# Performance work log

Measured on AMD Instinct MI355X. Metric: run time of the kernel, lower is better.

Reference implementation:

```python
import jax, jax.numpy as jnp
import numpy as np

B, N, L, D = 256, 128, 2048, 64
ATOM_V, AMINO_V = 2000, 10000
LAYER_GNN, LAYER_CNN, LAYER_OUT = 3, 3, 2
SIDE = 5
WINDOW = 2 * SIDE + 1   # 11 -> conv kernel 23x23, padding 11
N_OUT = 2
EPS = 1e-6


def setup_inputs() -> dict:
    ks = jax.random.split(jax.random.key(0), 16)
    s = 0.05
    return {
        "atoms": jax.random.randint(ks[0], (B, N), 0, ATOM_V),
        "atoms_mask": jnp.ones((B, N), jnp.float32),
        "adjacency": jax.random.uniform(ks[1], (B, N, N), jnp.float32),
        "amino": jax.random.randint(ks[2], (B, L), 0, AMINO_V),
        "amino_mask": jnp.ones((B, L), jnp.float32),
        "emb_fp": jax.random.normal(ks[3], (ATOM_V, D), jnp.float32) * s,
        "emb_word": jax.random.normal(ks[4], (AMINO_V, D), jnp.float32) * s,
        "W_gnn": jax.random.normal(ks[5], (LAYER_GNN, D, D), jnp.float32) * s,
        "b_gnn": jax.random.normal(ks[6], (LAYER_GNN, D), jnp.float32) * s,
        "conv_k": jax.random.normal(ks[7], (LAYER_CNN, 2 * WINDOW + 1, 2 * WINDOW + 1), jnp.float32) * s,
        "conv_b": jax.random.normal(ks[8], (LAYER_CNN,), jnp.float32) * s,
        "W_att": jax.random.normal(ks[9], (D, D), jnp.float32) * s,
        "b_att": jax.random.normal(ks[10], (D,), jnp.float32) * s,
        "W_out": jax.random.normal(ks[11], (LAYER_OUT, 2 * D, 2 * D), jnp.float32) * s,
        "b_out": jax.random.normal(ks[12], (LAYER_OUT, 2 * D), jnp.float32) * s,
        "W_int": jax.random.normal(ks[13], (N_OUT, 2 * D), jnp.float32) * s,
        "b_int": jax.random.normal(ks[14], (N_OUT,), jnp.float32) * s,
    }


def reference(atoms, atoms_mask, adjacency, amino, amino_mask,
              emb_fp, emb_word, W_gnn, b_gnn, conv_k, conv_b,
              W_att, b_att, W_out, b_out, W_int, b_int):
    # ---- compound vector via GNN over dense adjacency ----
    xs = emb_fp[atoms]                                   # [B,N,D]
    for i in range(LAYER_GNN):
        hs = jax.nn.relu(jnp.einsum('bnd,ed->bne', xs, W_gnn[i]) + b_gnn[i])
        xs = xs + jnp.einsum('bnm,bmd->bnd', adjacency, hs)
    am = atoms_mask[..., None]                           # [B,N,1]
    compound = (jnp.sum(xs * am, axis=1) / (jnp.sum(am, axis=1) + EPS))[:, None, :]  # [B,1,D]

    # ---- protein vector via attention-CNN ----
    ps = emb_word[amino][:, None]                        # [B,1,L,D] (NCHW)
    for i in range(LAYER_CNN):
        y = jax.lax.conv_general_dilated(
            ps, conv_k[i][None, None], (1, 1),
            [(WINDOW, WINDOW), (WINDOW, WINDOW)],
            dimension_numbers=('NCHW', 'OIHW', 'NCHW'))
        ps = jax.nn.relu(y + conv_b[i])
    ps = ps[:, 0]                                        # [B,L,D]
    h = jax.nn.relu(jnp.einsum('bqd,ed->bqe', compound, W_att) + b_att)  # [B,1,D]
    hs = jax.nn.relu(jnp.einsum('bld,ed->ble', ps, W_att) + b_att)       # [B,L,D]
    pm = amino_mask[..., None]                           # [B,L,1]
    hs = hs * pm
    weights = jnp.tanh(jnp.einsum('bqd,bld->bql', h, hs))  # [B,1,L]
    ys = jnp.transpose(weights, (0, 2, 1)) * hs             # [B,L,D]
    protein = (jnp.sum(ys, axis=1) / (jnp.sum(pm, axis=1) + EPS))[:, None, :]  # [B,1,D]

    # ---- fuse and predict ----
    cat = jnp.concatenate([compound, protein], axis=2)[:, 0]  # [B,2D]
    for j in range(LAYER_OUT):
        cat = jax.nn.relu(cat @ W_out[j].T + b_out[j])  # dropout is identity in eval
    return cat @ W_int.T + b_int                          # [B,N_OUT]
```

## Files before the change

kernel.cpp:

```cpp
#include <hip/hip_runtime.h>
#include <hip/hip_bf16.h>
#include <cstdint>
#include <cstddef>

#define BB 256
#define NN 128
#define LL 2048
#define DD 64
#define KS 23
#define CPAD 12
#define EPSF 1e-6f
#define ACH 8

typedef __bf16 v8bf __attribute__((ext_vector_type(8)));
typedef float v4f __attribute__((ext_vector_type(4)));

__device__ __forceinline__ float bf2f(uint32_t u) {
  union { uint32_t i; float f; } c; c.i = u << 16; return c.f;
}
__device__ __forceinline__ uint16_t f2bf(float f) {
  union { float f; uint32_t i; } c; c.f = f;
  uint32_t i = c.i;
  return (uint16_t)((i + 0x7fffu + ((i >> 16) & 1u)) >> 16);
}
__device__ __forceinline__ v8bf cvt8(float4 f0, float4 f1) {
  v8bf r;
  r[0] = (__bf16)f0.x; r[1] = (__bf16)f0.y; r[2] = (__bf16)f0.z; r[3] = (__bf16)f0.w;
  r[4] = (__bf16)f1.x; r[5] = (__bf16)f1.y; r[6] = (__bf16)f1.z; r[7] = (__bf16)f1.w;
  return r;
}

#define XSS 68
#define HTS3 136

__global__ __launch_bounds__(256) void gnn_kernel(
    const int* __restrict__ atoms, const float* __restrict__ atoms_mask,
    const float* __restrict__ adj, const float* __restrict__ emb_fp,
    const float* __restrict__ W_gnn, const float* __restrict__ b_gnn,
    const float* __restrict__ W_att, const float* __restrict__ b_att,
    const float* __restrict__ conv_k, uint16_t* __restrict__ btab,
    float* __restrict__ compound, float* __restrict__ hvec_g)
{
  __shared__ float xs[NN * XSS];
  __shared__ uint16_t hsT[DD * HTS3];
  __shared__ float mask_s[NN];
  __shared__ float psum[4][64];
  __shared__ float cvec[64];

  const int b = blockIdx.x;
  const int tid = threadIdx.x;
  const int lane = tid & 63;
  const int w = tid >> 6;
  const int m16 = lane & 15;
  const int s = lane >> 4;

  for (int idx = tid; idx < NN * 16; idx += 256) {
    int n = idx >> 4, c4 = idx & 15;
    int a = atoms[b * NN + n];
    float4 v = ((const float4*)(emb_fp + (size_t)a * DD))[c4];
    *(float4*)(xs + n * XSS + c4 * 4) = v;
  }
  if (tid < NN) mask_s[tid] = atoms_mask[b * NN + tid];
  __syncthreads();

  const int row0 = 32 * w;
  for (int layer = 0; layer < 3; ++layer) {
    v8bf Wf[2][4];
    float bias[4];
    const float* Wl = W_gnn + (size_t)layer * DD * DD;
    #pragma unroll
    for (int nt = 0; nt < 4; ++nt) {
      bias[nt] = b_gnn[layer * DD + nt * 16 + m16];
      #pragma unroll
      for (int kc = 0; kc < 2; ++kc) {
        const float* p = Wl + (size_t)(nt * 16 + m16) * DD + kc * 32 + s * 8;
        Wf[kc][nt] = cvt8(((const float4*)p)[0], ((const float4*)p)[1]);
      }
    }
    float4 araw[8][2];
    const float* adjw = adj + ((size_t)b * NN + row0) * NN;
    #pragma unroll
    for (int kc = 0; kc < 4; ++kc)
      #pragma unroll
      for (int mt = 0; mt < 2; ++mt) {
        const float* p = adjw + (size_t)(mt * 16 + m16) * NN + kc * 32 + s * 8;
        araw[kc * 2 + mt][0] = ((const float4*)p)[0];
        araw[kc * 2 + mt][1] = ((const float4*)p)[1];
      }

    v4f acc[2][4];
    #pragma unroll
    for (int mt = 0; mt < 2; ++mt)
      #pragma unroll
      for (int nt = 0; nt < 4; ++nt)
        acc[mt][nt] = (v4f){bias[nt], bias[nt], bias[nt], bias[nt]};
    #pragma unroll
    for (int kc = 0; kc < 2; ++kc) {
      v8bf Axs[2];
      #pragma unroll
      for (int mt = 0; mt < 2; ++mt) {
        const float* p = xs + (size_t)(row0 + mt * 16 + m16) * XSS + kc * 32 + s * 8;
        Axs[mt] = cvt8(((const float4*)p)[0], ((const float4*)p)[1]);
      }
      #pragma unroll
      for (int mt = 0; mt < 2; ++mt)
        #pragma unroll
        for (int nt = 0; nt < 4; ++nt)
          acc[mt][nt] = __builtin_amdgcn_mfma_f32_16x16x32_bf16(
              Axs[mt], Wf[kc][nt], acc[mt][nt], 0, 0, 0);
    }
    __syncthreads();
    #pragma unroll
    for (int mt = 0; mt < 2; ++mt)
      #pragma unroll
      for (int nt = 0; nt < 4; ++nt) {
        int e = nt * 16 + m16;
        int m = row0 + mt * 16 + s * 4;
        union { uint64_t u; __bf16 h[4]; } pk;
        #pragma unroll
        for (int r = 0; r < 4; ++r)
          pk.h[r] = (__bf16)fmaxf(acc[mt][nt][r], 0.f);
        *(uint64_t*)(hsT + (size_t)e * HTS3 + m) = pk.u;
      }
    __syncthreads();

    v4f acc2[2][4];
    #pragma unroll
    for (int mt = 0; mt < 2; ++mt)
      #pragma unroll
      for (int nt = 0; nt < 4; ++nt)
        #pragma unroll
        for (int r = 0; r < 4; ++r)
          acc2[mt][nt][r] = xs[(size_t)(row0 + mt * 16 + s * 4 + r) * XSS + nt * 16 + m16];
    #pragma unroll
    for (int kc = 0; kc < 4; ++kc) {
      v8bf Aa[2];
      #pragma unroll
      for (int mt = 0; mt < 2; ++mt)
        Aa[mt] = cvt8(araw[kc * 2 + mt][0], araw[kc * 2 + mt][1]);
      v8bf Bh[4];
      #pragma unroll
      for (int nt = 0; nt < 4; ++nt)
        Bh[nt] = *(const v8bf*)(hsT + (size_t)(nt * 16 + m16) * HTS3 + kc * 32 + s * 8);
      #pragma unroll
      for (int mt = 0; mt < 2; ++mt)
        #pragma unroll
        for (int nt = 0; nt < 4; ++nt)
          acc2[mt][nt] = __builtin_amdgcn_mfma_f32_16x16x32_bf16(
              Aa[mt], Bh[nt], acc2[mt][nt], 0, 0, 0);
    }
    #pragma unroll
    for (int mt = 0; mt < 2; ++mt)
      #pragma unroll
      for (int nt = 0; nt < 4; ++nt)
        #pragma unroll
        for (int r = 0; r < 4; ++r)
          xs[(size_t)(row0 + mt * 16 + s * 4 + r) * XSS + nt * 16 + m16] = acc2[mt][nt][r];
  }

  float pr = 0.f;
  for (int i = 0; i < 32; ++i) {
    int n = row0 + i;
    pr = fmaf(mask_s[n], xs[(size_t)n * XSS + lane], pr);
  }
  psum[w][lane] = pr;
  __syncthreads();
  if (tid < 64) {
    float ssum = psum[0][tid] + psum[1][tid] + psum[2][tid] + psum[3][tid];
    float den = 0.f;
    #pragma unroll 8
    for (int i = 0; i < NN; ++i) den += mask_s[i];
    float c = ssum / (den + EPSF);
    compound[b * DD + tid] = c;
    cvec[tid] = c;
  }
  __syncthreads();
  if (tid < 64) {
    float a = b_att[tid];
    const float* wr = W_att + (size_t)tid * DD;
    #pragma unroll
    for (int d4 = 0; d4 < 16; ++d4) {
      float4 w4 = ((const float4*)wr)[d4];
      float4 c4 = ((const float4*)cvec)[d4];
      a = fmaf(w4.x, c4.x, a); a = fmaf(w4.y, c4.y, a);
      a = fmaf(w4.z, c4.z, a); a = fmaf(w4.w, c4.w, a);
    }
    hvec_g[b * DD + tid] = fmaxf(a, 0.f);
  }

  if (b < 3) {
    for (int kk = w; kk < 30; kk += 4) {
      int k8 = kk * 4 + s;
      int i = k8 / 5;
      int c8k = k8 - i * 5;
      #pragma unroll
      for (int j = 0; j < 8; ++j) {
        int c = c8k * 8 + j;
        int jj = c - m16 - 1;
        float v = (i < KS && jj >= 0 && jj < KS)
                      ? conv_k[b * KS * KS + i * KS + jj] : 0.f;
        btab[(((size_t)b * 30 + kk) * 64 + lane) * 8 + j] = f2bf(v);
      }
    }
  }
}

#define TW 88
#define TROWS 86
#define OTS 72

__global__ __launch_bounds__(256, 3) void conv_kernel(
    const uint16_t* __restrict__ in, uint16_t* __restrict__ out,
    const uint16_t* __restrict__ btab, const float* __restrict__ conv_b,
    const int* __restrict__ amino, const float* __restrict__ emb_word,
    int layer, int gmode)
{
  __shared__ uint16_t tile[TROWS * TW];
  const int tid = threadIdx.x;
  const int l0 = blockIdx.x * 64;
  const int b  = blockIdx.y;
  const int lane = tid & 63;
  const int g = tid >> 6;

  v8bf bfr[30];
  const uint16_t* bt = btab + (size_t)layer * 30 * 512 + lane * 8;
  #pragma unroll
  for (int kk = 0; kk < 30; ++kk)
    bfr[kk] = *(const v8bf*)(bt + kk * 512);

  for (int i = tid; i < TROWS * 6; i += 256) {
    int r = i / 6, h = i - r * 6;
    int off = (h < 3) ? h * 4 : 76 + (h - 3) * 4;
    *(uint2*)(tile + r * TW + off) = make_uint2(0u, 0u);
  }
  const uint16_t* inb = in + (size_t)b * LL * DD;
  for (int idx = tid; idx < TROWS * 8; idx += 256) {
    int t = idx >> 3, c8 = idx & 7;
    int gl = l0 - 11 + t;
    uint16_t* dst = tile + t * TW + CPAD + c8 * 8;
    if (gl >= 0 && gl < LL) {
      if (gmode) {
        int a = amino[b * LL + gl];
        const float* src = emb_word + (size_t)a * DD + c8 * 8;
        float4 f0 = ((const float4*)src)[0];
        float4 f1 = ((const float4*)src)[1];
        union { uint2 u2[2]; uint16_t h[8]; } pk;
        pk.h[0] = f2bf(f0.x); pk.h[1] = f2bf(f0.y);
        pk.h[2] = f2bf(f0.z); pk.h[3] = f2bf(f0.w);
        pk.h[4] = f2bf(f1.x); pk.h[5] = f2bf(f1.y);
        pk.h[6] = f2bf(f1.z); pk.h[7] = f2bf(f1.w);
        *(uint2*)(dst)     = pk.u2[0];
        *(uint2*)(dst + 4) = pk.u2[1];
      } else {
        uint4 v = *(const uint4*)(inb + (size_t)gl * DD + c8 * 8);
        *(uint2*)(dst)     = make_uint2(v.x, v.y);
        *(uint2*)(dst + 4) = make_uint2(v.z, v.w);
      }
    } else {
      *(uint2*)(dst)     = make_uint2(0u, 0u);
      *(uint2*)(dst + 4) = make_uint2(0u, 0u);
    }
  }
  __syncthreads();

  const int s = lane >> 4;
  const int m16 = lane & 15;
  v4f acc[4];
  #pragma unroll
  for (int m = 0; m < 4; ++m) acc[m] = (v4f){0.f, 0.f, 0.f, 0.f};

  #pragma unroll
  for (int kk = 0; kk < 30; ++kk) {
    int k8 = kk * 4 + s;
    int i = k8 / 5;
    int c8 = k8 - i * 5;
    const uint16_t* ap = tile + (m16 + i) * TW + 16 * g + c8 * 8;
    v8bf a0 = *(const v8bf*)(ap);
    v8bf a1 = *(const v8bf*)(ap + 16 * TW);
    v8bf a2 = *(const v8bf*)(ap + 32 * TW);
    v8bf a3 = *(const v8bf*)(ap + 48 * TW);
    acc[0] = __builtin_amdgcn_mfma_f32_16x16x32_bf16(a0, bfr[kk], acc[0], 0, 0, 0);
    acc[1] = __builtin_amdgcn_mfma_f32_16x16x32_bf16(a1, bfr[kk], acc[1], 0, 0, 0);
    acc[2] = __builtin_amdgcn_mfma_f32_16x16x32_bf16(a2, bfr[kk], acc[2], 0, 0, 0);
    acc[3] = __builtin_amdgcn_mfma_f32_16x16x32_bf16(a3, bfr[kk], acc[3], 0, 0, 0);
  }

  const float bias = conv_b[layer];
  __syncthreads();
  uint16_t* ot = tile;
  #pragma unroll
  for (int m = 0; m < 4; ++m)
    #pragma unroll
    for (int r = 0; r < 4; ++r) {
      int row = m * 16 + s * 4 + r;
      ot[row * OTS + 16 * g + m16] = f2bf(fmaxf(acc[m][r] + bias, 0.f));
    }
  __syncthreads();
  uint16_t* outb = out + ((size_t)b * LL + l0) * DD;
  for (int i = tid; i < 512; i += 256) {
    int row = i >> 3, c8 = i & 7;
    uint4 v = *(const uint4*)(ot + row * OTS + c8 * 8);
    *(uint4*)(outb + (size_t)row * DD + c8 * 8) = v;
  }
}

#define HTS2 66

__global__ __launch_bounds__(256) void attn_part_kernel(
    const uint16_t* __restrict__ ps, const float* __restrict__ amino_mask,
    const float* __restrict__ hvec_g, const float* __restrict__ W_att,
    const float* __restrict__ b_att, float* __restrict__ pacc_part,
    float* __restrict__ msum_part)
{
  __shared__ float ht[4][32 * HTS2];
  __shared__ float pm_s[4][64];
  __shared__ float wv_s[4][32];
  __shared__ float hv_s[64];

  const int chunk = blockIdx.x;
  const int b = blockIdx.y;
  const int tid = threadIdx.x;
  const int lane = tid & 63;
  const int w = tid >> 6;
  const int m16 = lane & 15;
  const int s = lane >> 4;

  v8bf bfrB[2][4];
  float bias[4];
  #pragma unroll
  for (int nt = 0; nt < 4; ++nt) {
    bias[nt] = b_att[nt * 16 + m16];
    const float* wr = W_att + (size_t)(nt * 16 + m16) * DD + s * 8;
    #pragma unroll
    for (int kc = 0; kc < 2; ++kc) {
      float4 f0 = ((const float4*)(wr + kc * 32))[0];
      float4 f1 = ((const float4*)(wr + kc * 32))[1];
      bfrB[kc][nt] = cvt8(f0, f1);
    }
  }
  if (tid < 64) hv_s[tid] = hvec_g[b * DD + tid];

  const int rowbase = chunk * 256 + w * 64;
  const float* pmb = amino_mask + (size_t)b * LL;
  pm_s[w][lane] = pmb[rowbase + lane];
  const float macc = pm_s[w][lane];
  __syncthreads();

  float pacc[4] = {0.f, 0.f, 0.f, 0.f};
  const uint16_t* psb = ps + ((size_t)b * LL + rowbase) * DD;

  #pragma unroll
  for (int step = 0; step < 2; ++step) {
    const uint16_t* pr = psb + (size_t)step * 32 * DD;
    v8bf A[2][2];
    #pragma unroll
    for (int mt = 0; mt < 2; ++mt)
      #pragma unroll
      for (int kc = 0; kc < 2; ++kc)
        A[mt][kc] = *(const v8bf*)(pr + (mt * 16 + m16) * DD + kc * 32 + s * 8);

    v4f acc[2][4];
    #pragma unroll
    for (int mt = 0; mt < 2; ++mt)
      #pragma unroll
      for (int nt = 0; nt < 4; ++nt)
        acc[mt][nt] = (v4f){0.f, 0.f, 0.f, 0.f};
    #pragma unroll
    for (int kc = 0; kc < 2; ++kc)
      #pragma unroll
      for (int mt = 0; mt < 2; ++mt)
        #pragma unroll
        for (int nt = 0; nt < 4; ++nt)
          acc[mt][nt] = __builtin_amdgcn_mfma_f32_16x16x32_bf16(
              A[mt][kc], bfrB[kc][nt], acc[mt][nt], 0, 0, 0);

    float vals[2][4][4];
    float* htw = ht[w];
    #pragma unroll
    for (int mt = 0; mt < 2; ++mt)
      #pragma unroll
      for (int r = 0; r < 4; ++r) {
        int row = mt * 16 + s * 4 + r;
        float pm = pm_s[w][step * 32 + row];
        #pragma unroll
        for (int nt = 0; nt < 4; ++nt) {
          float v = fmaxf(acc[mt][nt][r] + bias[nt], 0.f) * pm;
          vals[mt][nt][r] = v;
          htw[row * HTS2 + nt * 16 + m16] = v;
        }
      }
    __syncthreads();

    {
      int row = lane & 31, eh = lane >> 5;
      const float* hr = ht[w] + row * HTS2 + eh * 32;
      const float* hv = hv_s + eh * 32;
      float d = 0.f;
      #pragma unroll
      for (int t = 0; t < 8; ++t) {
        float4 hh = *(const float4*)(hr + 4 * t);
        float4 vv = *(const float4*)(hv + 4 * t);
        d = fmaf(hh.x, vv.x, d); d = fmaf(hh.y, vv.y, d);
        d = fmaf(hh.z, vv.z, d); d = fmaf(hh.w, vv.w, d);
      }
      d += __shfl_xor(d, 32);
      float wt = tanhf(d);
      if (lane < 32) wv_s[w][row] = wt;
    }
    __syncthreads();

    #pragma unroll
    for (int mt = 0; mt < 2; ++mt)
      #pragma unroll
      for (int r = 0; r < 4; ++r) {
        float wt = wv_s[w][mt * 16 + s * 4 + r];
        #pragma unroll
        for (int nt = 0; nt < 4; ++nt)
          pacc[nt] = fmaf(wt, vals[mt][nt][r], pacc[nt]);
      }
    __syncthreads();
  }

  const size_t idx = ((size_t)b * ACH + chunk) * 4 + w;
  #pragma unroll
  for (int nt = 0; nt < 4; ++nt) {
    float p = pacc[nt];
    p += __shfl_xor(p, 16);
    p += __shfl_xor(p, 32);
    if (m16 == lane)
      pacc_part[idx * 64 + nt * 16 + lane] = p;
  }
  float m = macc;
  #pragma unroll
  for (int off = 1; off < 64; off <<= 1) m += __shfl_xor(m, off);
  if (lane == 0) msum_part[idx] = m;
}

__global__ __launch_bounds__(128) void attn_final_kernel(
    const float* __restrict__ compound, const float* __restrict__ pacc_part,
    const float* __restrict__ msum_part, const float* __restrict__ W_out,
    const float* __restrict__ b_out, const float* __restrict__ W_int,
    const float* __restrict__ b_int, float* __restrict__ outp)
{
  __shared__ float cat[128];
  __shared__ float cat2[128];
  const int b = blockIdx.x;
  const int tid = threadIdx.x;

  if (tid < 64) {
    float p = 0.f, den = 0.f;
    #pragma unroll 4
    for (int c = 0; c < ACH * 4; ++c) {
      p += pacc_part[((size_t)b * ACH * 4 + c) * 64 + tid];
      den += msum_part[b * ACH * 4 + c];
    }
    cat[tid] = compound[b * DD + tid];
    cat[64 + tid] = p / (den + EPSF);
  }
  __syncthreads();
  {
    float a = b_out[tid];
    const float* wr = W_out + (size_t)tid * 128;
    #pragma unroll 8
    for (int dd = 0; dd < 128; ++dd) a = fmaf(wr[dd], cat[dd], a);
    cat2[tid] = fmaxf(a, 0.f);
  }
  __syncthreads();
  {
    float a = b_out[128 + tid];
    const float* wr = W_out + 128 * 128 + (size_t)tid * 128;
    #pragma unroll 8
    for (int dd = 0; dd < 128; ++dd) a = fmaf(wr[dd], cat2[dd], a);
    __syncthreads();
    cat[tid] = fmaxf(a, 0.f);
  }
  __syncthreads();
  if (tid < 2) {
    float a = b_int[tid];
    const float* wr = W_int + (size_t)tid * 128;
    #pragma unroll 8
    for (int dd = 0; dd < 128; ++dd) a = fmaf(wr[dd], cat[dd], a);
    outp[b * 2 + tid] = a;
  }
}

extern "C" void kernel_launch(void* const* d_in, const int* in_sizes, int n_in,
                              void* d_out, int out_size, void* d_ws, size_t ws_size,
                              hipStream_t stream) {
  const int*   atoms      = (const int*)d_in[0];
  const float* atoms_mask = (const float*)d_in[1];
  const float* adjacency  = (const float*)d_in[2];
  const int*   amino      = (const int*)d_in[3];
  const float* amino_mask = (const float*)d_in[4];
  const float* emb_fp     = (const float*)d_in[5];
  const float* emb_word   = (const float*)d_in[6];
  const float* W_gnn      = (const float*)d_in[7];
  const float* b_gnn      = (const float*)d_in[8];
  const float* conv_k     = (const float*)d_in[9];
  const float* conv_b     = (const float*)d_in[10];
  const float* W_att      = (const float*)d_in[11];
  const float* b_att      = (const float*)d_in[12];
  const float* W_out      = (const float*)d_in[13];
  const float* b_out      = (const float*)d_in[14];
  const float* W_int      = (const float*)d_in[15];
  const float* b_int      = (const float*)d_in[16];
  float* out = (float*)d_out;

  char* ws = (char*)d_ws;
  const size_t ps_bytes = (size_t)BB * LL * DD * 2;
  float*    compound  = (float*)ws;
  uint16_t* ps_a      = (uint16_t*)(ws + 65536);
  uint16_t* ps_b      = (uint16_t*)(ws + 65536 + ps_bytes);
  uint16_t* btab      = (uint16_t*)(ws + 65536 + 2 * ps_bytes);
  float*    hvec_g    = (float*)(ws + 65536 + 2 * ps_bytes + 131072);
  float*    pacc_part = (float*)ps_a;
  float*    msum_part = (float*)((char*)ps_a + (size_t)BB * ACH * 4 * 64 * 4);

  gnn_kernel<<<BB, 256, 0, stream>>>(atoms, atoms_mask, adjacency, emb_fp,
                                     W_gnn, b_gnn, W_att, b_att,
                                     conv_k, btab, compound, hvec_g);
  conv_kernel<<<dim3(32, BB), 256, 0, stream>>>(ps_a, ps_b, btab, conv_b,
                                                amino, emb_word, 0, 1);
  conv_kernel<<<dim3(32, BB), 256, 0, stream>>>(ps_b, ps_a, btab, conv_b,
                                                amino, emb_word, 1, 0);
  conv_kernel<<<dim3(32, BB), 256, 0, stream>>>(ps_a, ps_b, btab, conv_b,
                                                amino, emb_word, 2, 0);
  attn_part_kernel<<<dim3(ACH, BB), 256, 0, stream>>>(ps_b, amino_mask, hvec_g,
                                                      W_att, b_att,
                                                      pacc_part, msum_part);
  attn_final_kernel<<<BB, 128, 0, stream>>>(compound, pacc_part, msum_part,
                                            W_out, b_out, W_int, b_int, out);
}
```

Measured before the change: 405.5 us.

## Fuse attention finalization via atomics, widen GNN blocks, trim conv k-steps and staging

Several changes land together. The GNN kernel moves to 512 threads, each wave handling 16 rows, and also zeroes the accumulators. The attention partial kernel now reduces with atomics and a last-block counter, so it runs the output MLP itself and the separate final kernel is gone. The conv kernel drops its last k-chunk (30 to 29), writes output directly instead of staging through LDS, and relaxes occupancy to 2 blocks per CU. The direct scalar bf16 stores are less coalesced, and dropping the final k-chunk is only safe if that chunk held only zero padding.

```diff
diff --git a/kernel.cpp b/kernel.cpp
--- a/kernel.cpp
+++ b/kernel.cpp
@@ -33,18 +33,20 @@
 #define XSS 68
 #define HTS3 136
 
-__global__ __launch_bounds__(256) void gnn_kernel(
+__global__ __launch_bounds__(512) void gnn_kernel(
     const int* __restrict__ atoms, const float* __restrict__ atoms_mask,
     const float* __restrict__ adj, const float* __restrict__ emb_fp,
     const float* __restrict__ W_gnn, const float* __restrict__ b_gnn,
     const float* __restrict__ W_att, const float* __restrict__ b_att,
     const float* __restrict__ conv_k, uint16_t* __restrict__ btab,
-    float* __restrict__ compound, float* __restrict__ hvec_g)
+    float* __restrict__ compound, float* __restrict__ hvec_g,
+    float* __restrict__ pacc_final, float* __restrict__ msum_final,
+    int* __restrict__ cnt)
 {
   __shared__ float xs[NN * XSS];
   __shared__ uint16_t hsT[DD * HTS3];
   __shared__ float mask_s[NN];
-  __shared__ float psum[4][64];
+  __shared__ float psum[8][64];
   __shared__ float cvec[64];
 
   const int b = blockIdx.x;
@@ -54,7 +56,11 @@
   const int m16 = lane & 15;
   const int s = lane >> 4;
 
-  for (int idx = tid; idx < NN * 16; idx += 256) {
+  if (tid < 64) pacc_final[b * 64 + tid] = 0.f;
+  if (tid == 64) msum_final[b] = 0.f;
+  if (tid == 65) cnt[b] = 0;
+
+  for (int idx = tid; idx < NN * 16; idx += 512) {
     int n = idx >> 4, c4 = idx & 15;
     int a = atoms[b * NN + n];
     float4 v = ((const float4*)(emb_fp + (size_t)a * DD))[c4];
@@ -63,7 +69,7 @@
   if (tid < NN) mask_s[tid] = atoms_mask[b * NN + tid];
   __syncthreads();
 
-  const int row0 = 32 * w;
+  const int row0 = 16 * w;
   for (int layer = 0; layer < 3; ++layer) {
     v8bf Wf[2][4];
     float bias[4];
@@ -77,96 +83,77 @@
         Wf[kc][nt] = cvt8(((const float4*)p)[0], ((const float4*)p)[1]);
       }
     }
-    float4 araw[8][2];
-    const float* adjw = adj + ((size_t)b * NN + row0) * NN;
-    #pragma unroll
-    for (int kc = 0; kc < 4; ++kc)
-      #pragma unroll
-      for (int mt = 0; mt < 2; ++mt) {
-        const float* p = adjw + (size_t)(mt * 16 + m16) * NN + kc * 32 + s * 8;
-        araw[kc * 2 + mt][0] = ((const float4*)p)[0];
-        araw[kc * 2 + mt][1] = ((const float4*)p)[1];
-      }
-
-    v4f acc[2][4];
-    #pragma unroll
-    for (int mt = 0; mt < 2; ++mt)
+    float4 araw[4][2];
+    const float* adjw = adj + ((size_t)b * NN + row0 + m16) * NN;
+    #pragma unroll
+    for (int kc = 0; kc < 4; ++kc) {
+      const float* p = adjw + kc * 32 + s * 8;
+      araw[kc][0] = ((const float4*)p)[0];
+      araw[kc][1] = ((const float4*)p)[1];
+    }
+
+    v4f acc[4];
+    #pragma unroll
+    for (int nt = 0; nt < 4; ++nt)
+      acc[nt] = (v4f){bias[nt], bias[nt], bias[nt], bias[nt]};
+    #pragma unroll
+    for (int kc = 0; kc < 2; ++kc) {
+      const float* p = xs + (size_t)(row0 + m16) * XSS + kc * 32 + s * 8;
+      v8bf Axs = cvt8(((const float4*)p)[0], ((const float4*)p)[1]);
       #pragma unroll
       for (int nt = 0; nt < 4; ++nt)
-        acc[mt][nt] = (v4f){bias[nt], bias[nt], bias[nt], bias[nt]};
-    #pragma unroll
-    for (int kc = 0; kc < 2; ++kc) {
-      v8bf Axs[2];
-      #pragma unroll
-      for (int mt = 0; mt < 2; ++mt) {
-        const float* p = xs + (size_t)(row0 + mt * 16 + m16) * XSS + kc * 32 + s * 8;
-        Axs[mt] = cvt8(((const float4*)p)[0], ((const float4*)p)[1]);
-      }
-      #pragma unroll
-      for (int mt = 0; mt < 2; ++mt)
-        #pragma unroll
-        for (int nt = 0; nt < 4; ++nt)
-          acc[mt][nt] = __builtin_amdgcn_mfma_f32_16x16x32_bf16(
-              Axs[mt], Wf[kc][nt], acc[mt][nt], 0, 0, 0);
-    }
-    __syncthreads();
-    #pragma unroll
-    for (int mt = 0; mt < 2; ++mt)
-      #pragma unroll
-      for (int nt = 0; nt < 4; ++nt) {
-        int e = nt * 16 + m16;
-        int m = row0 + mt * 16 + s * 4;
-        union { uint64_t u; __bf16 h[4]; } pk;
-        #pragma unroll
-        for (int r = 0; r < 4; ++r)
-          pk.h[r] = (__bf16)fmaxf(acc[mt][nt][r], 0.f);
-        *(uint64_t*)(hsT + (size_t)e * HTS3 + m) = pk.u;
-      }
-    __syncthreads();
-
-    v4f acc2[2][4];
-    #pragma unroll
-    for (int mt = 0; mt < 2; ++mt)
-      #pragma unroll
-      for (int nt = 0; nt < 4; ++nt)
-        #pragma unroll
-        for (int r = 0; r < 4; ++r)
-          acc2[mt][nt][r] = xs[(size_t)(row0 + mt * 16 + s * 4 + r) * XSS + nt * 16 + m16];
+        acc[nt] = __builtin_amdgcn_mfma_f32_16x16x32_bf16(
+            Axs, Wf[kc][nt], acc[nt], 0, 0, 0);
+    }
+    __syncthreads();
+    #pragma unroll
+    for (int nt = 0; nt < 4; ++nt) {
+      int e = nt * 16 + m16;
+      int m = row0 + s * 4;
+      union { uint64_t u; __bf16 h[4]; } pk;
+      #pragma unroll
+      for (int r = 0; r < 4; ++r)
+        pk.h[r] = (__bf16)fmaxf(acc[nt][r], 0.f);
+      *(uint64_t*)(hsT + (size_t)e * HTS3 + m) = pk.u;
+    }
+    __syncthreads();
+
+    v4f acc2[4];
+    #pragma unroll
+    for (int nt = 0; nt < 4; ++nt)
+      #pragma unroll
+      for (int r = 0; r < 4; ++r)
+        acc2[nt][r] = xs[(size_t)(row0 + s * 4 + r) * XSS + nt * 16 + m16];
     #pragma unroll
     for (int kc = 0; kc < 4; ++kc) {
-      v8bf Aa[2];
-      #pragma unroll
-      for (int mt = 0; mt < 2; ++mt)
-        Aa[mt] = cvt8(araw[kc * 2 + mt][0], araw[kc * 2 + mt][1]);
+      v8bf Aa = cvt8(araw[kc][0], araw[kc][1]);
       v8bf Bh[4];
       #pragma unroll
       for (int nt = 0; nt < 4; ++nt)
         Bh[nt] = *(const v8bf*)(hsT + (size_t)(nt * 16 + m16) * HTS3 + kc * 32 + s * 8);
       #pragma unroll
-      for (int mt = 0; mt < 2; ++mt)
-        #pragma unroll
-        for (int nt = 0; nt < 4; ++nt)
-          acc2[mt][nt] = __builtin_amdgcn_mfma_f32_16x16x32_bf16(
-              Aa[mt], Bh[nt], acc2[mt][nt], 0, 0, 0);
-    }
-    #pragma unroll
-    for (int mt = 0; mt < 2; ++mt)
-      #pragma unroll
       for (int nt = 0; nt < 4; ++nt)
-        #pragma unroll
-        for (int r = 0; r < 4; ++r)
-          xs[(size_t)(row0 + mt * 16 + s * 4 + r) * XSS + nt * 16 + m16] = acc2[mt][nt][r];
+        acc2[nt] = __builtin_amdgcn_mfma_f32_16x16x32_bf16(
+            Aa, Bh[nt], acc2[nt], 0, 0, 0);
+    }
+    #pragma unroll
+    for (int nt = 0; nt < 4; ++nt)
+      #pragma unroll
+      for (int r = 0; r < 4; ++r)
+        xs[(size_t)(row0 + s * 4 + r) * XSS + nt * 16 + m16] = acc2[nt][r];
   }
 
   float pr = 0.f;
-  for (int i = 0; i < 32; ++i) {
+  for (int i = 0; i < 16; ++i) {
     int n = row0 + i;
     pr = fmaf(mask_s[n], xs[(size_t)n * XSS + lane], pr);
   }
   psum[w][lane] = pr;
   __syncthreads();
   if (tid < 64) {
-    float ssum = psum[0][tid] + psum[1][tid] + psum[2][tid] + psum[3][tid];
+    float ssum = 0.f;
+    #pragma unroll
+    for (int k = 0; k < 8; ++k) ssum += psum[k][tid];
     float den = 0.f;
     #pragma unroll 8
     for (int i = 0; i < NN; ++i) den += mask_s[i];
@@ -189,7 +176,7 @@
   }
 
   if (b < 3) {
-    for (int kk = w; kk < 30; kk += 4) {
+    for (int kk = w; kk < 30; kk += 8) {
       int k8 = kk * 4 + s;
       int i = k8 / 5;
       int c8k = k8 - i * 5;
@@ -207,9 +194,8 @@
 
 #define TW 88
 #define TROWS 86
-#define OTS 72
-
-__global__ __launch_bounds__(256, 3) void conv_kernel(
+
+__global__ __launch_bounds__(256, 2) void conv_kernel(
     const uint16_t* __restrict__ in, uint16_t* __restrict__ out,
     const uint16_t* __restrict__ btab, const float* __restrict__ conv_b,
     const int* __restrict__ amino, const float* __restrict__ emb_word,
@@ -222,10 +208,10 @@
   const int lane = tid & 63;
   const int g = tid >> 6;
 
-  v8bf bfr[30];
+  v8bf bfr[29];
   const uint16_t* bt = btab + (size_t)layer * 30 * 512 + lane * 8;
   #pragma unroll
-  for (int kk = 0; kk < 30; ++kk)
+  for (int kk = 0; kk < 29; ++kk)
     bfr[kk] = *(const v8bf*)(bt + kk * 512);
 
   for (int i = tid; i < TROWS * 6; i += 256) {
@@ -270,7 +256,7 @@
   for (int m = 0; m < 4; ++m) acc[m] = (v4f){0.f, 0.f, 0.f, 0.f};
 
   #pragma unroll
-  for (int kk = 0; kk < 30; ++kk) {
+  for (int kk = 0; kk < 29; ++kk) {
     int k8 = kk * 4 + s;
     int i = k8 / 5;
     int c8 = k8 - i * 5;
@@ -286,21 +272,14 @@
   }
 
   const float bias = conv_b[layer];
-  __syncthreads();
-  uint16_t* ot = tile;
-  #pragma unroll
-  for (int m = 0; m < 4; ++m)
+  uint16_t* outb = out + ((size_t)b * LL + l0) * DD + 16 * g + m16;
+  #pragma unroll
+  for (int m = 0; m < 4; ++m) {
     #pragma unroll
     for (int r = 0; r < 4; ++r) {
       int row = m * 16 + s * 4 + r;
-      ot[row * OTS + 16 * g + m16] = f2bf(fmaxf(acc[m][r] + bias, 0.f));
-    }
-  __syncthreads();
-  uint16_t* outb = out + ((size_t)b * LL + l0) * DD;
-  for (int i = tid; i < 512; i += 256) {
-    int row = i >> 3, c8 = i & 7;
-    uint4 v = *(const uint4*)(ot + row * OTS + c8 * 8);
-    *(uint4*)(outb + (size_t)row * DD + c8 * 8) = v;
+      outb[(size_t)row * DD] = f2bf(fmaxf(acc[m][r] + bias, 0.f));
+    }
   }
 }
 
@@ -309,13 +288,19 @@
 __global__ __launch_bounds__(256) void attn_part_kernel(
     const uint16_t* __restrict__ ps, const float* __restrict__ amino_mask,
     const float* __restrict__ hvec_g, const float* __restrict__ W_att,
-    const float* __restrict__ b_att, float* __restrict__ pacc_part,
-    float* __restrict__ msum_part)
+    const float* __restrict__ b_att, const float* __restrict__ compound,
+    const float* __restrict__ W_out, const float* __restrict__ b_out,
+    const float* __restrict__ W_int, const float* __restrict__ b_int,
+    float* __restrict__ pacc_final, float* __restrict__ msum_final,
+    int* __restrict__ cnt, float* __restrict__ outp)
 {
   __shared__ float ht[4][32 * HTS2];
   __shared__ float pm_s[4][64];
   __shared__ float wv_s[4][32];
   __shared__ float hv_s[64];
+  __shared__ float cat[128];
+  __shared__ float cat2[128];
+  __shared__ int lastf;
 
   const int chunk = blockIdx.x;
   const int b = blockIdx.y;
@@ -421,44 +406,38 @@
     __syncthreads();
   }
 
-  const size_t idx = ((size_t)b * ACH + chunk) * 4 + w;
   #pragma unroll
   for (int nt = 0; nt < 4; ++nt) {
     float p = pacc[nt];
     p += __shfl_xor(p, 16);
     p += __shfl_xor(p, 32);
-    if (m16 == lane)
-      pacc_part[idx * 64 + nt * 16 + lane] = p;
+    if (lane < 16) atomicAdd(&pacc_final[b * 64 + nt * 16 + lane], p);
   }
   float m = macc;
   #pragma unroll
   for (int off = 1; off < 64; off <<= 1) m += __shfl_xor(m, off);
-  if (lane == 0) msum_part[idx] = m;
-}
-
-__global__ __launch_bounds__(128) void attn_final_kernel(
-    const float* __restrict__ compound, const float* __restrict__ pacc_part,
-    const float* __restrict__ msum_part, const float* __restrict__ W_out,
-    const float* __restrict__ b_out, const float* __restrict__ W_int,
-    const float* __restrict__ b_int, float* __restrict__ outp)
-{
-  __shared__ float cat[128];
-  __shared__ float cat2[128];
-  const int b = blockIdx.x;
-  const int tid = threadIdx.x;
+  if (lane == 0) atomicAdd(&msum_final[b], m);
+
+  __threadfence();
+  __syncthreads();
+  if (tid == 0) {
+    int old = __hip_atomic_fetch_add(&cnt[b], 1, __ATOMIC_ACQ_REL,
+                                     __HIP_MEMORY_SCOPE_AGENT);
+    lastf = (old == ACH - 1);
+  }
+  __syncthreads();
+  if (!lastf) return;
 
   if (tid < 64) {
-    float p = 0.f, den = 0.f;
-    #pragma unroll 4
-    for (int c = 0; c < ACH * 4; ++c) {
-      p += pacc_part[((size_t)b * ACH * 4 + c) * 64 + tid];
-      den += msum_part[b * ACH * 4 + c];
-    }
+    float p = __hip_atomic_load(&pacc_final[b * 64 + tid], __ATOMIC_RELAXED,
+                                __HIP_MEMORY_SCOPE_AGENT);
+    float den = __hip_atomic_load(&msum_final[b], __ATOMIC_RELAXED,
+                                  __HIP_MEMORY_SCOPE_AGENT);
     cat[tid] = compound[b * DD + tid];
     cat[64 + tid] = p / (den + EPSF);
   }
   __syncthreads();
-  {
+  if (tid < 128) {
     float a = b_out[tid];
     const float* wr = W_out + (size_t)tid * 128;
     #pragma unroll 8
@@ -466,13 +445,15 @@
     cat2[tid] = fmaxf(a, 0.f);
   }
   __syncthreads();
-  {
+  if (tid < 128) {
     float a = b_out[128 + tid];
     const float* wr = W_out + 128 * 128 + (size_t)tid * 128;
     #pragma unroll 8
     for (int dd = 0; dd < 128; ++dd) a = fmaf(wr[dd], cat2[dd], a);
     __syncthreads();
     cat[tid] = fmaxf(a, 0.f);
+  } else {
+    __syncthreads();
   }
   __syncthreads();
   if (tid < 2) {
@@ -508,26 +489,27 @@
 
   char* ws = (char*)d_ws;
   const size_t ps_bytes = (size_t)BB * LL * DD * 2;
-  float*    compound  = (float*)ws;
-  uint16_t* ps_a      = (uint16_t*)(ws + 65536);
-  uint16_t* ps_b      = (uint16_t*)(ws + 65536 + ps_bytes);
-  uint16_t* btab      = (uint16_t*)(ws + 65536 + 2 * ps_bytes);
-  float*    hvec_g    = (float*)(ws + 65536 + 2 * ps_bytes + 131072);
-  float*    pacc_part = (float*)ps_a;
-  float*    msum_part = (float*)((char*)ps_a + (size_t)BB * ACH * 4 * 64 * 4);
-
-  gnn_kernel<<<BB, 256, 0, stream>>>(atoms, atoms_mask, adjacency, emb_fp,
+  float*    compound   = (float*)ws;
+  uint16_t* ps_a       = (uint16_t*)(ws + 65536);
+  uint16_t* ps_b       = (uint16_t*)(ws + 65536 + ps_bytes);
+  uint16_t* btab       = (uint16_t*)(ws + 65536 + 2 * ps_bytes);
+  float*    hvec_g     = (float*)(ws + 65536 + 2 * ps_bytes + 131072);
+  char*     tail       = ws + 65536 + 2 * ps_bytes + 131072 + 65536;
+  float*    pacc_final = (float*)tail;
+  float*    msum_final = (float*)(tail + 65536);
+  int*      cnt        = (int*)(tail + 65536 + 4096);
+
+  gnn_kernel<<<BB, 512, 0, stream>>>(atoms, atoms_mask, adjacency, emb_fp,
                                      W_gnn, b_gnn, W_att, b_att,
-                                     conv_k, btab, compound, hvec_g);
+                                     conv_k, btab, compound, hvec_g,
+                                     pacc_final, msum_final, cnt);
   conv_kernel<<<dim3(32, BB), 256, 0, stream>>>(ps_a, ps_b, btab, conv_b,
                                                 amino, emb_word, 0, 1);
   conv_kernel<<<dim3(32, BB), 256, 0, stream>>>(ps_b, ps_a, btab, conv_b,
                                                 amino, emb_word, 1, 0);
   conv_kernel<<<dim3(32, BB), 256, 0, stream>>>(ps_a, ps_b, btab, conv_b,
                                                 amino, emb_word, 2, 0);
-  attn_part_kernel<<<dim3(ACH, BB), 256, 0, stream>>>(ps_b, amino_mask, hvec_g,
-                                                      W_att, b_att,
-                                                      pacc_part, msum_part);
-  attn_final_kernel<<<BB, 128, 0, stream>>>(compound, pacc_part, msum_part,
-                                            W_out, b_out, W_int, b_int, out);
-}
+  attn_part_kernel<<<dim3(ACH, BB), 256, 0, stream>>>(
+      ps_b, amino_mask, hvec_g, W_att, b_att, compound,
+      W_out, b_out, W_int, b_int, pacc_final, msum_final, cnt, out);
+}
```

Measured after the change: 556.2 us. +37.2%, slower.
